# Kernel optimization log

Hardware: AMD Instinct MI355X
Metric: run time of the kernel (lower is better)

## Reference

```python
import jax, jax.numpy as jnp
import numpy as np

N_NODES = 50000
N_EDGES = 600000
IN_DIM, HID, OUT_DIM = 128, 128, 64


def setup_inputs() -> dict:
    key = jax.random.key(0)
    ks = jax.random.split(key, 12)
    h = jax.random.normal(ks[0], (N_NODES, IN_DIM), dtype=jnp.float32)
    src = jax.random.randint(ks[1], (N_EDGES,), 0, N_NODES, dtype=jnp.int32)
    dst = jax.random.randint(ks[2], (N_EDGES,), 0, N_NODES, dtype=jnp.int32)
    dims = [(IN_DIM, HID), (HID, HID), (HID, HID), (HID, OUT_DIM)]
    params = {}
    for i, (di, do) in enumerate(dims):
        scale = 1.0 / np.sqrt(di)
        params[f"W{i}"] = jax.random.uniform(ks[3 + i], (di, do), jnp.float32, -scale, scale)
        params[f"b{i}"] = jnp.zeros((do,), jnp.float32)
    return dict(h=h, src=src, dst=dst, **params)


def _gcn_layer(h, W, b, src, dst, norm_src, norm_dst, n_nodes):
    # DGL GraphConv, norm='both': D^{-1/2} A D^{-1/2} (h W) + b
    x = (h * norm_src) @ W              # [N, out]
    agg = jax.ops.segment_sum(x[src], dst, num_segments=n_nodes)
    return agg * norm_dst + b


def reference(h, src, dst, W0, b0, W1, b1, W2, b2, W3, b3):
    n = h.shape[0]
    ones = jnp.ones((src.shape[0],), h.dtype)
    deg_out = jnp.clip(jax.ops.segment_sum(ones, src, num_segments=n), 1.0)
    deg_in = jnp.clip(jax.ops.segment_sum(ones, dst, num_segments=n), 1.0)
    norm_src = (deg_out ** -0.5)[:, None]
    norm_dst = (deg_in ** -0.5)[:, None]
    Ws = [(W0, b0), (W1, b1), (W2, b2), (W3, b3)]
    for i, (W, b) in enumerate(Ws):
        h = _gcn_layer(h, W, b, src, dst, norm_src, norm_dst, n)
        if i != len(Ws) - 1:
            h = jax.nn.relu(h)  # dropout is identity in eval mode
    return h
```

## Files before the change

### kernel.cpp

```cpp
#include <hip/hip_runtime.h>


namespace {

constexpr int NN = 50000;
constexpr int NE = 600000;
constexpr int SCAN_BLK = 256;
constexpr int NBLK = (NN + SCAN_BLK - 1) / SCAN_BLK;
constexpr int DEG_BLOCKS = 256;
constexpr int GEMM_TILES = (NN + 63) / 64;
constexpr int WCVT_ELEMS = 128 * 128 + 128 * 128 + 128 * 64;
constexpr int WCVT_BLOCKS = WCVT_ELEMS / 256;

typedef unsigned short bhalf;
typedef __attribute__((ext_vector_type(8))) short short8v;
typedef __attribute__((ext_vector_type(4))) float f32x4;

__device__ inline float blo(unsigned int v) {
  return __uint_as_float(v << 16);
}
__device__ inline float bhi(unsigned int v) {
  return __uint_as_float(v & 0xFFFF0000u);
}
__device__ inline unsigned int f2b_bits(float f) {
  unsigned int b = __float_as_uint(f);
  return b + 0x7FFFu + ((b >> 16) & 1u);
}
__device__ inline unsigned int pack2(float lo, float hi) {
  return (f2b_bits(lo) >> 16) | (f2b_bits(hi) & 0xFFFF0000u);
}
__device__ inline bhalf f2b(float f) { return (bhalf)(f2b_bits(f) >> 16); }

__global__ __launch_bounds__(SCAN_BLK) void scan1_norm_wcvt(
    const int* __restrict__ dego, const int* __restrict__ degi,
    int* __restrict__ bsum, float* __restrict__ ns, float* __restrict__ nd,
    const float* __restrict__ W1, const float* __restrict__ W2,
    const float* __restrict__ W3, bhalf* __restrict__ wt1,
    bhalf* __restrict__ wt2, bhalf* __restrict__ wt3) {
  if (blockIdx.x >= NBLK) {
    int flat = (blockIdx.x - NBLK) * 256 + threadIdx.x;
    if (flat < 16384) {
      int j = flat >> 7, k = flat & 127;
      wt1[flat] = f2b(W1[k * 128 + j]);
    } else if (flat < 32768) {
      int f = flat - 16384;
      int j = f >> 7, k = f & 127;
      wt2[f] = f2b(W2[k * 128 + j]);
    } else {
      int f = flat - 32768;
      int j = f >> 7, k = f & 127;
      wt3[f] = f2b(W3[k * 64 + j]);
    }
    return;
  }
  __shared__ int ws[SCAN_BLK / 64];
  int i = blockIdx.x * SCAN_BLK + threadIdx.x;
  int v = 0;
  if (i < NN) {
    int din = degi[i];
    int dout = dego[i];
    v = din;
    int a = dout < 1 ? 1 : dout;
    int b = din < 1 ? 1 : din;
    ns[i] = 1.0f / sqrtf((float)a);
    nd[i] = 1.0f / sqrtf((float)b);
  }
#pragma unroll
  for (int off = 32; off; off >>= 1) v += __shfl_down(v, off, 64);
  int lane = threadIdx.x & 63, w = threadIdx.x >> 6;
  if (lane == 0) ws[w] = v;
  __syncthreads();
  if (threadIdx.x == 0) {
    int s = 0;
#pragma unroll
    for (int k = 0; k < SCAN_BLK / 64; ++k) s += ws[k];
    bsum[blockIdx.x] = s;
  }
}

__global__ __launch_bounds__(256) void scan_phase2(const int* __restrict__ bsum,
                                                   int* __restrict__ bpre,
                                                   int* __restrict__ rowptr) {
  __shared__ int s[256];
  int t = threadIdx.x;
  int v = (t < NBLK) ? bsum[t] : 0;
  s[t] = v;
  __syncthreads();
  for (int off = 1; off < 256; off <<= 1) {
    int u = (t >= off) ? s[t - off] : 0;
    __syncthreads();
    s[t] += u;
    __syncthreads();
  }
  if (t < NBLK) bpre[t] = s[t] - v;
  if (t == 255) rowptr[NN] = s[255];
}

__global__ __launch_bounds__(SCAN_BLK) void scan_phase3(const int* __restrict__ deg,
                                                        const int* __restrict__ bpre,
                                                        int* __restrict__ rowptr) {
  __shared__ int s[SCAN_BLK];
  int t = threadIdx.x;
  int i = blockIdx.x * SCAN_BLK + t;
  int v = (i < NN) ? deg[i] : 0;
  s[t] = v;
  __syncthreads();
  for (int off = 1; off < SCAN_BLK; off <<= 1) {
    int u = (t >= off) ? s[t - off] : 0;
    __syncthreads();
    s[t] += u;
    __syncthreads();
  }
  if (i < NN) rowptr[i] = bpre[blockIdx.x] + s[t] - v;
}

__global__ void scatter_kernel(const int* __restrict__ src, const int* __restrict__ dst,
                               const int* __restrict__ le, const int* __restrict__ rowptr,
                               int* __restrict__ col) {
  int e = blockIdx.x * blockDim.x + threadIdx.x;
  if (e < NE) col[rowptr[dst[e]] + le[e]] = src[e];
}

__device__ void gemm0_body(const float* __restrict__ h, const float* __restrict__ W,
                           bhalf* __restrict__ x, int row0, float* hs, float* wl) {
  const int tid = threadIdx.x;
#pragma unroll
  for (int it = 0; it < 8; ++it) {
    int flat = it * 256 + tid;
    int row = flat >> 5;
    int c = flat & 31;
    int grow = row0 + row;
    float4 hv = make_float4(0.f, 0.f, 0.f, 0.f);
    if (grow < NN)
      hv = *reinterpret_cast<const float4*>(&h[(size_t)grow * 128 + c * 4]);
    float* d = &hs[row * 132 + c * 4];
    d[0] = hv.x; d[1] = hv.y; d[2] = hv.z; d[3] = hv.w;
  }

  const int rq = tid >> 4;
  const int cq = tid & 15;

  for (int ch = 0; ch < 2; ++ch) {
    __syncthreads();
#pragma unroll
    for (int it = 0; it < 8; ++it) {
      int flat = it * 256 + tid;
      int k = flat >> 4;
      int c4 = flat & 15;
      *reinterpret_cast<float4*>(&wl[k * 64 + c4 * 4]) =
          *reinterpret_cast<const float4*>(&W[k * 128 + ch * 64 + c4 * 4]);
    }
    __syncthreads();

    float acc[4][4] = {{0.f}};
#pragma unroll 4
    for (int k4 = 0; k4 < 32; ++k4) {
      float hv[4][4], wv[4][4];
#pragma unroll
      for (int i = 0; i < 4; ++i) {
        float4 t = *reinterpret_cast<const float4*>(&hs[(rq * 4 + i) * 132 + k4 * 4]);
        hv[i][0] = t.x; hv[i][1] = t.y; hv[i][2] = t.z; hv[i][3] = t.w;
      }
#pragma unroll
      for (int kk = 0; kk < 4; ++kk) {
        float4 t = *reinterpret_cast<const float4*>(&wl[(k4 * 4 + kk) * 64 + cq * 4]);
        wv[kk][0] = t.x; wv[kk][1] = t.y; wv[kk][2] = t.z; wv[kk][3] = t.w;
      }
#pragma unroll
      for (int i = 0; i < 4; ++i)
#pragma unroll
        for (int kk = 0; kk < 4; ++kk)
#pragma unroll
          for (int j = 0; j < 4; ++j)
            acc[i][j] = fmaf(hv[i][kk], wv[kk][j], acc[i][j]);
    }

#pragma unroll
    for (int i = 0; i < 4; ++i) {
      int row = row0 + rq * 4 + i;
      if (row < NN) {
        uint2 p;
        p.x = pack2(acc[i][0], acc[i][1]);
        p.y = pack2(acc[i][2], acc[i][3]);
        *reinterpret_cast<uint2*>(&x[(size_t)row * 128 + ch * 64 + cq * 4]) = p;
      }
    }
  }
}

__global__ __launch_bounds__(256, 2) void gemm0_deg_kernel(
    const float* __restrict__ h, const float* __restrict__ W,
    bhalf* __restrict__ x,
    const int* __restrict__ src, const int* __restrict__ dst,
    int* __restrict__ dego, int* __restrict__ degi, int* __restrict__ le) {
  __shared__ __align__(16) float hs[64 * 132];
  __shared__ __align__(16) float wl[128 * 64];
  if (blockIdx.x < DEG_BLOCKS) {
    const int stride = DEG_BLOCKS * 256;
    for (int e = blockIdx.x * 256 + threadIdx.x; e < NE; e += stride) {
      atomicAdd(&dego[src[e]], 1);
      le[e] = atomicAdd(&degi[dst[e]], 1);
    }
    return;
  }
  gemm0_body(h, W, x, (blockIdx.x - DEG_BLOCKS) * 64, hs, wl);
}

template <int DO>
__global__ __launch_bounds__(256, 2) void gemm_mfma(const bhalf* __restrict__ h,
                                                    const bhalf* __restrict__ wt,
                                                    const float* __restrict__ ns,
                                                    bhalf* __restrict__ x) {
  constexpr int CF = DO / 16;
  const int lane = threadIdx.x & 63;
  const int wv = threadIdx.x >> 6;
  const int tile = blockIdx.x * 4 + wv;
  if (tile >= NN / 16) return;
  const int row0 = tile * 16;
  const size_t arow = (size_t)(row0 + (lane & 15)) * 128;
  const int koff = (lane >> 4) * 8;
  const int bcol = lane & 15;

  f32x4 acc[CF];
#pragma unroll
  for (int cf = 0; cf < CF; ++cf) acc[cf] = (f32x4){0.f, 0.f, 0.f, 0.f};

#pragma unroll
  for (int ks = 0; ks < 4; ++ks) {
    const int k0 = ks * 32 + koff;
    short8v av = *reinterpret_cast<const short8v*>(&h[arow + k0]);
#pragma unroll
    for (int cf = 0; cf < CF; ++cf) {
      short8v bv = *reinterpret_cast<const short8v*>(
          &wt[(size_t)(cf * 16 + bcol) * 128 + k0]);
      acc[cf] = __builtin_amdgcn_mfma_f32_16x16x32_bf16(av, bv, acc[cf], 0, 0, 0);
    }
  }

  const int crow = row0 + ((lane >> 4) << 2);
  float nsv[4];
#pragma unroll
  for (int r = 0; r < 4; ++r) nsv[r] = ns[crow + r];
#pragma unroll
  for (int cf = 0; cf < CF; ++cf) {
#pragma unroll
    for (int r = 0; r < 4; ++r) {
      x[(size_t)(crow + r) * DO + cf * 16 + bcol] = f2b(acc[cf][r] * nsv[r]);
    }
  }
}

template <int D, bool RELU, bool NSRC, bool OUTBF>
__global__ __launch_bounds__(256) void gather2_kernel(const bhalf* __restrict__ x,
                                                      const int* __restrict__ rowptr,
                                                      const int* __restrict__ col,
                                                      const float* __restrict__ nd,
                                                      const float* __restrict__ b,
                                                      const float* __restrict__ nsv,
                                                      void* __restrict__ outp) {
  constexpr int LPR = D / 8;
  constexpr int EPW = 64 / LPR;
  const int wid = (blockIdx.x * blockDim.x + threadIdx.x) >> 6;
  const int lane = threadIdx.x & 63;
  const int n0 = wid * 2;
  if (n0 >= NN) return;
  const int n1 = n0 + 1;
  const int sub = lane / LPR;
  const int ci = (lane % LPR) * 8;
  const int beg0 = rowptr[n0], end0 = rowptr[n0 + 1];
  const int beg1 = rowptr[n1], end1 = rowptr[n1 + 1];
  int e0 = beg0 + sub;
  int e1 = beg1 + sub;
  const int d0 = end0 - beg0, d1 = end1 - beg1;
  const int iters = ((d0 > d1 ? d0 : d1) + EPW - 1) / EPW;

  float a0[8], a1[8];
#pragma unroll
  for (int k = 0; k < 8; ++k) { a0[k] = 0.f; a1[k] = 0.f; }

#pragma unroll 2
  for (int it = 0; it < iters; ++it) {
    const bool p0 = e0 < end0;
    const bool p1 = e1 < end1;
    const int ee0 = p0 ? e0 : 0;
    const int ee1 = p1 ? e1 : 0;
    const int c0 = col[ee0];
    const int c1 = col[ee1];
    const float s0 = p0 ? (NSRC ? nsv[c0] : 1.0f) : 0.0f;
    const float s1 = p1 ? (NSRC ? nsv[c1] : 1.0f) : 0.0f;
    const uint4 v0 = *reinterpret_cast<const uint4*>(&x[(size_t)c0 * D + ci]);
    const uint4 v1 = *reinterpret_cast<const uint4*>(&x[(size_t)c1 * D + ci]);
    float f0[8], f1[8];
    f0[0] = blo(v0.x); f0[1] = bhi(v0.x); f0[2] = blo(v0.y); f0[3] = bhi(v0.y);
    f0[4] = blo(v0.z); f0[5] = bhi(v0.z); f0[6] = blo(v0.w); f0[7] = bhi(v0.w);
    f1[0] = blo(v1.x); f1[1] = bhi(v1.x); f1[2] = blo(v1.y); f1[3] = bhi(v1.y);
    f1[4] = blo(v1.z); f1[5] = bhi(v1.z); f1[6] = blo(v1.w); f1[7] = bhi(v1.w);
#pragma unroll
    for (int k = 0; k < 8; ++k) {
      a0[k] = fmaf(s0, f0[k], a0[k]);
      a1[k] = fmaf(s1, f1[k], a1[k]);
    }
    e0 += EPW;
    e1 += EPW;
  }

#pragma unroll
  for (int off = LPR; off < 64; off <<= 1) {
#pragma unroll
    for (int k = 0; k < 8; ++k) {
      a0[k] += __shfl_xor(a0[k], off, 64);
      a1[k] += __shfl_xor(a1[k], off, 64);
    }
  }

  if (lane < 2 * LPR) {
    const bool g0 = lane < LPR;
    const int n = g0 ? n0 : n1;
    const int cw = (g0 ? lane : lane - LPR) * 8;
    const float* acc = g0 ? a0 : a1;
    const float s = nd[n];
    float4 b0 = *reinterpret_cast<const float4*>(&b[cw]);
    float4 b1 = *reinterpret_cast<const float4*>(&b[cw + 4]);
    float r[8];
    r[0] = fmaf(acc[0], s, b0.x); r[1] = fmaf(acc[1], s, b0.y);
    r[2] = fmaf(acc[2], s, b0.z); r[3] = fmaf(acc[3], s, b0.w);
    r[4] = fmaf(acc[4], s, b1.x); r[5] = fmaf(acc[5], s, b1.y);
    r[6] = fmaf(acc[6], s, b1.z); r[7] = fmaf(acc[7], s, b1.w);
    if (RELU) {
#pragma unroll
      for (int k = 0; k < 8; ++k) r[k] = fmaxf(r[k], 0.f);
    }
    if constexpr (OUTBF) {
      bhalf* out = (bhalf*)outp;
      uint4 p;
      p.x = pack2(r[0], r[1]);
      p.y = pack2(r[2], r[3]);
      p.z = pack2(r[4], r[5]);
      p.w = pack2(r[6], r[7]);
      *reinterpret_cast<uint4*>(&out[(size_t)n * D + cw]) = p;
    } else {
      float* out = (float*)outp;
      *reinterpret_cast<float4*>(&out[(size_t)n * D + cw]) =
          make_float4(r[0], r[1], r[2], r[3]);
      *reinterpret_cast<float4*>(&out[(size_t)n * D + cw + 4]) =
          make_float4(r[4], r[5], r[6], r[7]);
    }
  }
}

}

extern "C" void kernel_launch(void* const* d_in, const int* in_sizes, int n_in,
                              void* d_out, int out_size, void* d_ws, size_t ws_size,
                              hipStream_t stream) {
  const float* h0  = (const float*)d_in[0];
  const int*   src = (const int*)d_in[1];
  const int*   dst = (const int*)d_in[2];
  const float* W0 = (const float*)d_in[3];
  const float* b0 = (const float*)d_in[4];
  const float* W1 = (const float*)d_in[5];
  const float* b1 = (const float*)d_in[6];
  const float* W2 = (const float*)d_in[7];
  const float* b2 = (const float*)d_in[8];
  const float* W3 = (const float*)d_in[9];
  const float* b3 = (const float*)d_in[10];
  float* out = (float*)d_out;

  char* w = (char*)d_ws;
  size_t off = 0;
  auto take = [&](size_t bytes) {
    char* p = w + off;
    off = (off + bytes + 255) & ~size_t(255);
    return p;
  };
  int*   deg_out = (int*)take(NN * 4);
  int*   deg_in  = (int*)take(NN * 4);
  float* nsrc    = (float*)take(NN * 4);
  float* ndst    = (float*)take(NN * 4);
  int*   rowptr  = (int*)take((NN + 1) * 4);
  int*   le      = (int*)take(NE * 4);
  int*   col     = (int*)take(NE * 4);
  int*   bsum    = (int*)take(NBLK * 4);
  int*   bpre    = (int*)take(NBLK * 4);
  bhalf* xbuf    = (bhalf*)take((size_t)NN * 128 * 2);
  bhalf* hbuf    = (bhalf*)take((size_t)NN * 128 * 2);
  bhalf* wt1     = (bhalf*)take(128 * 128 * 2);
  bhalf* wt2     = (bhalf*)take(128 * 128 * 2);
  bhalf* wt3     = (bhalf*)take(64 * 128 * 2);
  (void)ws_size; (void)in_sizes; (void)n_in; (void)out_size;

  hipMemsetAsync(deg_out, 0, (size_t)((char*)nsrc - (char*)deg_out), stream);

  const int EB = (NE + 255) / 256;

  gemm0_deg_kernel<<<DEG_BLOCKS + GEMM_TILES, 256, 0, stream>>>(
      h0, W0, xbuf, src, dst, deg_out, deg_in, le);
  scan1_norm_wcvt<<<NBLK + WCVT_BLOCKS, SCAN_BLK, 0, stream>>>(
      deg_out, deg_in, bsum, nsrc, ndst, W1, W2, W3, wt1, wt2, wt3);
  scan_phase2<<<1, 256, 0, stream>>>(bsum, bpre, rowptr);
  scan_phase3<<<NBLK, SCAN_BLK, 0, stream>>>(deg_in, bpre, rowptr);
  scatter_kernel<<<EB, 256, 0, stream>>>(src, dst, le, rowptr, col);

  const int GATHER_BLOCKS = (NN / 2 * 64 + 255) / 256;
  const int MFMA_BLOCKS = (NN / 16 + 3) / 4;

  gather2_kernel<128, true, true, true><<<GATHER_BLOCKS, 256, 0, stream>>>(
      xbuf, rowptr, col, ndst, b0, nsrc, hbuf);
  gemm_mfma<128><<<MFMA_BLOCKS, 256, 0, stream>>>(hbuf, wt1, nsrc, xbuf);
  gather2_kernel<128, true, false, true><<<GATHER_BLOCKS, 256, 0, stream>>>(
      xbuf, rowptr, col, ndst, b1, nullptr, hbuf);
  gemm_mfma<128><<<MFMA_BLOCKS, 256, 0, stream>>>(hbuf, wt2, nsrc, xbuf);
  gather2_kernel<128, true, false, true><<<GATHER_BLOCKS, 256, 0, stream>>>(
      xbuf, rowptr, col, ndst, b2, nullptr, hbuf);
  gemm_mfma<64><<<MFMA_BLOCKS, 256, 0, stream>>>(hbuf, wt3, nsrc, xbuf);
  gather2_kernel<64, false, false, false><<<GATHER_BLOCKS, 256, 0, stream>>>(
      xbuf, rowptr, col, ndst, b3, nullptr, out);
}
```

Baseline: 250.5 us.

## Use bf16 MFMA for first-layer GEMM and merge scan phases two and three

```diff
diff --git a/kernel.cpp b/kernel.cpp
--- a/kernel.cpp
+++ b/kernel.cpp
@@ -7,9 +7,9 @@
 constexpr int NE = 600000;
 constexpr int SCAN_BLK = 256;
 constexpr int NBLK = (NN + SCAN_BLK - 1) / SCAN_BLK;
-constexpr int DEG_BLOCKS = 256;
-constexpr int GEMM_TILES = (NN + 63) / 64;
-constexpr int WCVT_ELEMS = 128 * 128 + 128 * 128 + 128 * 64;
+constexpr int EB = (NE + 255) / 256;
+constexpr int MFMA0_BLOCKS = (NN / 16 + 3) / 4;
+constexpr int WCVT_ELEMS = 16384 * 3 + 8192;
 constexpr int WCVT_BLOCKS = WCVT_ELEMS / 256;
 
 typedef unsigned short bhalf;
@@ -31,28 +31,89 @@
 }
 __device__ inline bhalf f2b(float f) { return (bhalf)(f2b_bits(f) >> 16); }
 
-__global__ __launch_bounds__(SCAN_BLK) void scan1_norm_wcvt(
-    const int* __restrict__ dego, const int* __restrict__ degi,
-    int* __restrict__ bsum, float* __restrict__ ns, float* __restrict__ nd,
-    const float* __restrict__ W1, const float* __restrict__ W2,
-    const float* __restrict__ W3, bhalf* __restrict__ wt1,
+__global__ __launch_bounds__(256) void wcvt_kernel(
+    const float* __restrict__ W0, const float* __restrict__ W1,
+    const float* __restrict__ W2, const float* __restrict__ W3,
+    bhalf* __restrict__ wt0, bhalf* __restrict__ wt1,
     bhalf* __restrict__ wt2, bhalf* __restrict__ wt3) {
-  if (blockIdx.x >= NBLK) {
-    int flat = (blockIdx.x - NBLK) * 256 + threadIdx.x;
-    if (flat < 16384) {
-      int j = flat >> 7, k = flat & 127;
-      wt1[flat] = f2b(W1[k * 128 + j]);
-    } else if (flat < 32768) {
-      int f = flat - 16384;
-      int j = f >> 7, k = f & 127;
-      wt2[f] = f2b(W2[k * 128 + j]);
-    } else {
-      int f = flat - 32768;
-      int j = f >> 7, k = f & 127;
-      wt3[f] = f2b(W3[k * 64 + j]);
+  int flat = blockIdx.x * 256 + threadIdx.x;
+  if (flat < 16384) {
+    int j = flat >> 7, k = flat & 127;
+    wt0[flat] = f2b(W0[k * 128 + j]);
+  } else if (flat < 32768) {
+    int f = flat - 16384;
+    int j = f >> 7, k = f & 127;
+    wt1[f] = f2b(W1[k * 128 + j]);
+  } else if (flat < 49152) {
+    int f = flat - 32768;
+    int j = f >> 7, k = f & 127;
+    wt2[f] = f2b(W2[k * 128 + j]);
+  } else {
+    int f = flat - 49152;
+    int j = f >> 7, k = f & 127;
+    wt3[f] = f2b(W3[k * 64 + j]);
+  }
+}
+
+__global__ __launch_bounds__(256, 4) void deg_gemm0_kernel(
+    const int* __restrict__ src, const int* __restrict__ dst,
+    int* __restrict__ dego, int* __restrict__ degi, int* __restrict__ le,
+    const float* __restrict__ h, const bhalf* __restrict__ wt0,
+    bhalf* __restrict__ x) {
+  if (blockIdx.x < EB) {
+    int e = blockIdx.x * 256 + threadIdx.x;
+    if (e < NE) {
+      atomicAdd(&dego[src[e]], 1);
+      le[e] = atomicAdd(&degi[dst[e]], 1);
     }
     return;
   }
+  const int lane = threadIdx.x & 63;
+  const int wv = threadIdx.x >> 6;
+  const int tile = (blockIdx.x - EB) * 4 + wv;
+  if (tile >= NN / 16) return;
+  const int row0 = tile * 16;
+  const size_t arow = (size_t)(row0 + (lane & 15)) * 128;
+  const int koff = (lane >> 4) * 8;
+  const int bcol = lane & 15;
+
+  f32x4 acc[8];
+#pragma unroll
+  for (int cf = 0; cf < 8; ++cf) acc[cf] = (f32x4){0.f, 0.f, 0.f, 0.f};
+
+#pragma unroll
+  for (int ks = 0; ks < 4; ++ks) {
+    const int k0 = ks * 32 + koff;
+    float4 ha = *reinterpret_cast<const float4*>(&h[arow + k0]);
+    float4 hb = *reinterpret_cast<const float4*>(&h[arow + k0 + 4]);
+    short8v av;
+    av[0] = (short)f2b(ha.x); av[1] = (short)f2b(ha.y);
+    av[2] = (short)f2b(ha.z); av[3] = (short)f2b(ha.w);
+    av[4] = (short)f2b(hb.x); av[5] = (short)f2b(hb.y);
+    av[6] = (short)f2b(hb.z); av[7] = (short)f2b(hb.w);
+#pragma unroll
+    for (int cf = 0; cf < 8; ++cf) {
+      short8v bv = *reinterpret_cast<const short8v*>(
+          &wt0[(size_t)(cf * 16 + bcol) * 128 + k0]);
+      acc[cf] = __builtin_amdgcn_mfma_f32_16x16x32_bf16(av, bv, acc[cf], 0, 0, 0);
+    }
+  }
+
+  const int crow = row0 + ((lane >> 4) << 2);
+#pragma unroll
+  for (int cf = 0; cf < 8; ++cf) {
+#pragma unroll
+    for (int r = 0; r < 4; ++r) {
+      x[(size_t)(crow + r) * 128 + cf * 16 + bcol] = f2b(acc[cf][r]);
+    }
+  }
+}
+
+__global__ __launch_bounds__(SCAN_BLK) void scan1_norm(const int* __restrict__ dego,
+                                                       const int* __restrict__ degi,
+                                                       int* __restrict__ bsum,
+                                                       float* __restrict__ ns,
+                                                       float* __restrict__ nd) {
   __shared__ int ws[SCAN_BLK / 64];
   int i = blockIdx.x * SCAN_BLK + threadIdx.x;
   int v = 0;
@@ -78,29 +139,24 @@
   }
 }
 
-__global__ __launch_bounds__(256) void scan_phase2(const int* __restrict__ bsum,
-                                                   int* __restrict__ bpre,
+__global__ __launch_bounds__(SCAN_BLK) void scan23(const int* __restrict__ deg,
+                                                   const int* __restrict__ bsum,
                                                    int* __restrict__ rowptr) {
-  __shared__ int s[256];
-  int t = threadIdx.x;
-  int v = (t < NBLK) ? bsum[t] : 0;
-  s[t] = v;
+  __shared__ int sb[SCAN_BLK];
+  __shared__ int s[SCAN_BLK];
+  const int t = threadIdx.x;
+  int vb = (t < NBLK) ? bsum[t] : 0;
+  sb[t] = vb;
   __syncthreads();
-  for (int off = 1; off < 256; off <<= 1) {
-    int u = (t >= off) ? s[t - off] : 0;
+  for (int off = 1; off < SCAN_BLK; off <<= 1) {
+    int u = (t >= off) ? sb[t - off] : 0;
     __syncthreads();
-    s[t] += u;
+    sb[t] += u;
     __syncthreads();
   }
-  if (t < NBLK) bpre[t] = s[t] - v;
-  if (t == 255) rowptr[NN] = s[255];
-}
-
-__global__ __launch_bounds__(SCAN_BLK) void scan_phase3(const int* __restrict__ deg,
-                                                        const int* __restrict__ bpre,
-                                                        int* __restrict__ rowptr) {
-  __shared__ int s[SCAN_BLK];
-  int t = threadIdx.x;
+  const int pre = (blockIdx.x == 0) ? 0 : sb[blockIdx.x - 1];
+  if (blockIdx.x == NBLK - 1 && t == 0) rowptr[NN] = sb[NBLK - 1];
+
   int i = blockIdx.x * SCAN_BLK + t;
   int v = (i < NN) ? deg[i] : 0;
   s[t] = v;
@@ -111,7 +167,7 @@
     s[t] += u;
     __syncthreads();
   }
-  if (i < NN) rowptr[i] = bpre[blockIdx.x] + s[t] - v;
+  if (i < NN) rowptr[i] = pre + s[t] - v;
 }
 
 __global__ void scatter_kernel(const int* __restrict__ src, const int* __restrict__ dst,
@@ -119,91 +175,6 @@
                                int* __restrict__ col) {
   int e = blockIdx.x * blockDim.x + threadIdx.x;
   if (e < NE) col[rowptr[dst[e]] + le[e]] = src[e];
-}
-
-__device__ void gemm0_body(const float* __restrict__ h, const float* __restrict__ W,
-                           bhalf* __restrict__ x, int row0, float* hs, float* wl) {
-  const int tid = threadIdx.x;
-#pragma unroll
-  for (int it = 0; it < 8; ++it) {
-    int flat = it * 256 + tid;
-    int row = flat >> 5;
-    int c = flat & 31;
-    int grow = row0 + row;
-    float4 hv = make_float4(0.f, 0.f, 0.f, 0.f);
-    if (grow < NN)
-      hv = *reinterpret_cast<const float4*>(&h[(size_t)grow * 128 + c * 4]);
-    float* d = &hs[row * 132 + c * 4];
-    d[0] = hv.x; d[1] = hv.y; d[2] = hv.z; d[3] = hv.w;
-  }
-
-  const int rq = tid >> 4;
-  const int cq = tid & 15;
-
-  for (int ch = 0; ch < 2; ++ch) {
-    __syncthreads();
-#pragma unroll
-    for (int it = 0; it < 8; ++it) {
-      int flat = it * 256 + tid;
-      int k = flat >> 4;
-      int c4 = flat & 15;
-      *reinterpret_cast<float4*>(&wl[k * 64 + c4 * 4]) =
-          *reinterpret_cast<const float4*>(&W[k * 128 + ch * 64 + c4 * 4]);
-    }
-    __syncthreads();
-
-    float acc[4][4] = {{0.f}};
-#pragma unroll 4
-    for (int k4 = 0; k4 < 32; ++k4) {
-      float hv[4][4], wv[4][4];
-#pragma unroll
-      for (int i = 0; i < 4; ++i) {
-        float4 t = *reinterpret_cast<const float4*>(&hs[(rq * 4 + i) * 132 + k4 * 4]);
-        hv[i][0] = t.x; hv[i][1] = t.y; hv[i][2] = t.z; hv[i][3] = t.w;
-      }
-#pragma unroll
-      for (int kk = 0; kk < 4; ++kk) {
-        float4 t = *reinterpret_cast<const float4*>(&wl[(k4 * 4 + kk) * 64 + cq * 4]);
-        wv[kk][0] = t.x; wv[kk][1] = t.y; wv[kk][2] = t.z; wv[kk][3] = t.w;
-      }
-#pragma unroll
-      for (int i = 0; i < 4; ++i)
-#pragma unroll
-        for (int kk = 0; kk < 4; ++kk)
-#pragma unroll
-          for (int j = 0; j < 4; ++j)
-            acc[i][j] = fmaf(hv[i][kk], wv[kk][j], acc[i][j]);
-    }
-
-#pragma unroll
-    for (int i = 0; i < 4; ++i) {
-      int row = row0 + rq * 4 + i;
-      if (row < NN) {
-        uint2 p;
-        p.x = pack2(acc[i][0], acc[i][1]);
-        p.y = pack2(acc[i][2], acc[i][3]);
-        *reinterpret_cast<uint2*>(&x[(size_t)row * 128 + ch * 64 + cq * 4]) = p;
-      }
-    }
-  }
-}
-
-__global__ __launch_bounds__(256, 2) void gemm0_deg_kernel(
-    const float* __restrict__ h, const float* __restrict__ W,
-    bhalf* __restrict__ x,
-    const int* __restrict__ src, const int* __restrict__ dst,
-    int* __restrict__ dego, int* __restrict__ degi, int* __restrict__ le) {
-  __shared__ __align__(16) float hs[64 * 132];
-  __shared__ __align__(16) float wl[128 * 64];
-  if (blockIdx.x < DEG_BLOCKS) {
-    const int stride = DEG_BLOCKS * 256;
-    for (int e = blockIdx.x * 256 + threadIdx.x; e < NE; e += stride) {
-      atomicAdd(&dego[src[e]], 1);
-      le[e] = atomicAdd(&degi[dst[e]], 1);
-    }
-    return;
-  }
-  gemm0_body(h, W, x, (blockIdx.x - DEG_BLOCKS) * 64, hs, wl);
 }
 
 template <int DO>
@@ -381,9 +352,9 @@
   int*   le      = (int*)take(NE * 4);
   int*   col     = (int*)take(NE * 4);
   int*   bsum    = (int*)take(NBLK * 4);
-  int*   bpre    = (int*)take(NBLK * 4);
   bhalf* xbuf    = (bhalf*)take((size_t)NN * 128 * 2);
   bhalf* hbuf    = (bhalf*)take((size_t)NN * 128 * 2);
+  bhalf* wt0     = (bhalf*)take(128 * 128 * 2);
   bhalf* wt1     = (bhalf*)take(128 * 128 * 2);
   bhalf* wt2     = (bhalf*)take(128 * 128 * 2);
   bhalf* wt3     = (bhalf*)take(64 * 128 * 2);
@@ -391,14 +362,11 @@
 
   hipMemsetAsync(deg_out, 0, (size_t)((char*)nsrc - (char*)deg_out), stream);
 
-  const int EB = (NE + 255) / 256;
-
-  gemm0_deg_kernel<<<DEG_BLOCKS + GEMM_TILES, 256, 0, stream>>>(
-      h0, W0, xbuf, src, dst, deg_out, deg_in, le);
-  scan1_norm_wcvt<<<NBLK + WCVT_BLOCKS, SCAN_BLK, 0, stream>>>(
-      deg_out, deg_in, bsum, nsrc, ndst, W1, W2, W3, wt1, wt2, wt3);
-  scan_phase2<<<1, 256, 0, stream>>>(bsum, bpre, rowptr);
-  scan_phase3<<<NBLK, SCAN_BLK, 0, stream>>>(deg_in, bpre, rowptr);
+  wcvt_kernel<<<WCVT_BLOCKS, 256, 0, stream>>>(W0, W1, W2, W3, wt0, wt1, wt2, wt3);
+  deg_gemm0_kernel<<<EB + MFMA0_BLOCKS, 256, 0, stream>>>(
+      src, dst, deg_out, deg_in, le, h0, wt0, xbuf);
+  scan1_norm<<<NBLK, SCAN_BLK, 0, stream>>>(deg_out, deg_in, bsum, nsrc, ndst);
+  scan23<<<NBLK, SCAN_BLK, 0, stream>>>(deg_in, bsum, rowptr);
   scatter_kernel<<<EB, 256, 0, stream>>>(src, dst, le, rowptr, col);
 
   const int GATHER_BLOCKS = (NN / 2 * 64 + 255) / 256;
```

Result: no change. 249.9 us (-0.2%).
